# Performance work log

Measured on AMD Instinct MI355X. Metric: run time of the kernel, lower is better.

## Reference

```python
import jax, jax.numpy as jnp
import numpy as np

B, C, L, H = 2, 512, 4096, 8
D = C // H  # depth per head


def setup_inputs() -> dict:
    key = jax.random.key(0)
    k1, k2, k3 = jax.random.split(key, 3)
    queries = jax.random.normal(k1, (B, C, L), dtype=jnp.float32)
    mask = jnp.ones((B, L), dtype=jnp.int32)
    # xavier-ish scaling for stability
    Wm = jax.random.normal(k2, (2 * C, C), dtype=jnp.float32) * (1.0 / np.sqrt(C))
    Wq = jax.random.normal(k3, (C, C), dtype=jnp.float32) * (1.0 / np.sqrt(C))
    return {"queries": queries, "mask": mask, "Wm": Wm, "Wq": Wq}


def reference(queries, mask, Wm, Wq):
    # 1x1 conv projections == channel matmuls on [B, C, L]
    q = jnp.einsum('oc,bcl->bol', Wq, queries)   # [B, C, L]
    m = jnp.einsum('oc,bcl->bol', Wm, queries)   # [B, 2C, L]
    # to [B, L, *], split heads -> [B, H, L, D]
    qh = q.transpose(0, 2, 1).reshape(B, L, H, D).transpose(0, 2, 1, 3)
    mem = m.transpose(0, 2, 1)                   # [B, L, 2C]
    k, v = jnp.split(mem, 2, axis=2)             # each [B, L, C]
    kh = k.reshape(B, L, H, D).transpose(0, 2, 1, 3)
    vh = v.reshape(B, L, H, D).transpose(0, 2, 1, 3)
    qh = qh * (D ** -0.5)
    logits = jnp.einsum('bhqd,bhkd->bhqk', qh, kh)          # [B, H, L, L]
    mf = mask.astype(jnp.float32)[:, None, None, :]          # [B, 1, 1, L]
    logits = logits + (-1e30) * (1.0 - mf)
    weights = jax.nn.softmax(logits, axis=-1)                # dropout is identity in eval
    out = jnp.einsum('bhqk,bhkd->bhqd', weights, vh)         # [B, H, L, D]
    # combine heads -> [B, L, C] -> [B, C, L]
    return out.transpose(0, 2, 1, 3).reshape(B, L, C).transpose(0, 2, 1)
```

## Files before the change

### kernel.cpp

```cpp
#include <hip/hip_runtime.h>

#define Bn 2
#define Cn 512
#define Ln 4096
#define Hn 8
#define Dn 64

typedef _Float16 f16;
typedef _Float16 h8 __attribute__((ext_vector_type(8)));
typedef _Float16 h4 __attribute__((ext_vector_type(4)));
typedef float f32x4 __attribute__((ext_vector_type(4)));
typedef float f32x16 __attribute__((ext_vector_type(16)));

#define MFMA32(a, b, c) __builtin_amdgcn_mfma_f32_16x16x32_f16(a, b, c, 0, 0, 0)
#define MFMA3216(a, b, c) __builtin_amdgcn_mfma_f32_32x32x16_f16(a, b, c, 0, 0, 0)
#define AS1(p) ((const __attribute__((address_space(1))) void*)(p))
#define AS3(p) ((__attribute__((address_space(3))) void*)(p))

__global__ __launch_bounds__(256) void k_transpose(const float* __restrict__ X,
                                                   f16* __restrict__ Xt) {
  int bid = blockIdx.x;
  int b  = bid >> 9;
  int r  = bid & 511;
  int lt = r >> 3, ct = r & 7;
  int l0 = lt << 6, c0 = ct << 6;
  __shared__ f16 t[64][66];
  int tid = threadIdx.x;
  int lx = tid & 63, cg = tid >> 6;
  const float* xb = X + ((size_t)b * Cn) * Ln;
#pragma unroll
  for (int rr = 0; rr < 16; ++rr) {
    int cl = cg * 16 + rr;
    t[lx][cl] = (f16)xb[(size_t)(c0 + cl) * Ln + l0 + lx];
  }
  __syncthreads();
  f16* xo = Xt + ((size_t)b * Ln + l0) * Cn + c0;
  int cx = tid & 63, lg = tid >> 6;
#pragma unroll
  for (int rr = 0; rr < 16; ++rr) {
    int ll = lg * 16 + rr;
    xo[(size_t)ll * Cn + cx] = t[ll][cx];
  }
}

__global__ __launch_bounds__(256) void k_proj(const float* __restrict__ Wq,
                                              const float* __restrict__ Wm,
                                              const f16* __restrict__ Xt,
                                              f16* __restrict__ Qd,
                                              f16* __restrict__ Kd,
                                              f16* __restrict__ Vv) {
  int bid = blockIdx.x;
  int b = bid / 384;
  int r = bid % 384;
  int mt = r >> 5, nt = r & 31;
  int o0 = mt << 7, l0 = nt << 7;
  __shared__ f16 a_lds[128][40];
  __shared__ f16 b_lds[128][40];
  int tid = threadIdx.x;
  int lane = tid & 63, w = tid >> 6;
  int wr = w >> 1, wc = w & 1;
  f32x4 acc[4][4] = {};

  int sr = tid >> 1;
  int scg = (tid & 1) << 4;
  int o_s = o0 + sr;
  const float* wrow = (o_s < 512) ? (Wq + (size_t)o_s * Cn)
                                  : (Wm + (size_t)(o_s - 512) * Cn);
  const f16* xrow = Xt + ((size_t)b * Ln + l0 + sr) * Cn;

  for (int kt = 0; kt < 16; ++kt) {
    int c0 = kt << 5;
    __syncthreads();
#pragma unroll
    for (int i = 0; i < 4; ++i) {
      float4 w4 = *(const float4*)(wrow + c0 + scg + 4 * i);
      h4 hh = { (f16)w4.x, (f16)w4.y, (f16)w4.z, (f16)w4.w };
      *(h4*)&a_lds[sr][scg + 4 * i] = hh;
    }
#pragma unroll
    for (int i = 0; i < 2; ++i)
      *(h8*)&b_lds[sr][scg + 8 * i] = *(const h8*)(xrow + c0 + scg + 8 * i);
    __syncthreads();

    h8 af[4], bf[4];
#pragma unroll
    for (int mi = 0; mi < 4; ++mi)
      af[mi] = *(const h8*)&a_lds[wr * 64 + mi * 16 + (lane & 15)][(lane >> 4) * 8];
#pragma unroll
    for (int ni = 0; ni < 4; ++ni)
      bf[ni] = *(const h8*)&b_lds[wc * 64 + ni * 16 + (lane & 15)][(lane >> 4) * 8];
#pragma unroll
    for (int mi = 0; mi < 4; ++mi)
#pragma unroll
      for (int ni = 0; ni < 4; ++ni)
        acc[mi][ni] = MFMA32(af[mi], bf[ni], acc[mi][ni]);
  }

  const float QSCALE = 0.18033688011112042f;
  int lrow = (lane >> 4) << 2;
  int lcol = lane & 15;
#pragma unroll
  for (int mi = 0; mi < 4; ++mi) {
    int ob = o0 + wr * 64 + mi * 16 + lrow;
#pragma unroll
    for (int ni = 0; ni < 4; ++ni) {
      int lc = l0 + wc * 64 + ni * 16 + lcol;
      f32x4 a = acc[mi][ni];
      if (ob < 512) {
        int h = ob >> 6, d = ob & 63;
        h4 hh = { (f16)(a[0] * QSCALE), (f16)(a[1] * QSCALE),
                  (f16)(a[2] * QSCALE), (f16)(a[3] * QSCALE) };
        *(h4*)&Qd[(((size_t)b * Hn + h) * Ln + lc) * Dn + d] = hh;
      } else if (ob < 1024) {
        int oc = ob - 512;
        int h = oc >> 6, d = oc & 63;
        h4 hh = { (f16)a[0], (f16)a[1], (f16)a[2], (f16)a[3] };
        *(h4*)&Kd[(((size_t)b * Hn + h) * Ln + lc) * Dn + d] = hh;
      } else {
        int oc = ob - 1024;
#pragma unroll
        for (int rr = 0; rr < 4; ++rr)
          Vv[((size_t)b * Cn + oc + rr) * Ln + lc] = (f16)a[rr];
      }
    }
  }
}

__global__ __launch_bounds__(256, 2) void k_attn(const f16* __restrict__ Qd,
                                                 const f16* __restrict__ Kd,
                                                 const f16* __restrict__ Vv,
                                                 const int* __restrict__ mask,
                                                 float* __restrict__ out) {
  int bid0 = blockIdx.x;
  int bid = (bid0 & 7) * 64 + (bid0 >> 3);
  int bh = bid >> 5, ib = bid & 31;
  int b = bh >> 3, h = bh & 7;
  int tid = threadIdx.x;
  int lane = tid & 63, w = tid >> 6;
  int il = lane & 31, hi = lane >> 5;

  __shared__ __align__(16) f16 kbuf[4][64 * 64];
  __shared__ __align__(16) f16 vbuf[4][64 * 64];

  int qb = ib * 128 + w * 32;
  const f16* qp = Qd + ((size_t)bh * Ln + qb + il) * Dn;
  h8 qreg[4];
#pragma unroll
  for (int dt = 0; dt < 4; ++dt)
    qreg[dt] = *(const h8*)(qp + dt * 16 + hi * 8);

  const int* mbase = mask + (size_t)b * Ln;
  unsigned long long flags;
  {
    const int4* mp = (const int4*)mbase + lane * 16;
    int ac = 1;
#pragma unroll
    for (int q = 0; q < 16; ++q) { int4 v = mp[q]; ac &= v.x & v.y & v.z & v.w; }
    flags = __ballot(ac == 1);
  }

  const f16* kbase = Kd + (size_t)bh * Ln * Dn;
  const f16* vbase = Vv + ((size_t)b * Cn + h * 64) * Ln;
  int koff[2], voff[2];
#pragma unroll
  for (int q = 0; q < 2; ++q) {
    int rr = w * 16 + q * 8 + (lane >> 3);
    int swz = (lane & 7) ^ (rr & 7);
    koff[q] = rr * 64 + swz * 8;
    voff[q] = rr * Ln + swz * 8;
  }

#define STAGE(bi, t)                                                            \
  {                                                                             \
    _Pragma("unroll")                                                           \
    for (int q = 0; q < 2; ++q) {                                               \
      __builtin_amdgcn_global_load_lds(AS1(kbase + (size_t)(t) * 4096 + koff[q]),\
                                       AS3(&kbuf[bi][(w * 16 + q * 8) * 64]),   \
                                       16, 0, 0);                               \
      __builtin_amdgcn_global_load_lds(AS1(vbase + (size_t)(t) * 64 + voff[q]), \
                                       AS3(&vbuf[bi][(w * 16 + q * 8) * 64]),   \
                                       16, 0, 0);                               \
    }                                                                           \
  }

  f32x16 acc0 = {}, acc1 = {};
  float mrow = -1e38f;
  float lsum = 0.f;
  int swz7 = il & 7;

#define QK_TILE(KL, SN0, SN1)                                    \
  {                                                              \
    const f16* kl_ = (KL);                                       \
    f32x16 z0 = {}, z1 = {};                                     \
    _Pragma("unroll")                                            \
    for (int dt = 0; dt < 4; ++dt) {                             \
      int c = ((dt * 2 + hi) ^ swz7) << 3;                       \
      h8 ak0 = *(const h8*)&kl_[il * 64 + c];                    \
      h8 ak1 = *(const h8*)&kl_[(32 + il) * 64 + c];             \
      z0 = MFMA3216(ak0, qreg[dt], z0);                          \
      z1 = MFMA3216(ak1, qreg[dt], z1);                          \
    }                                                            \
    SN0 = z0; SN1 = z1;                                          \
  }

#define MASK_FIX(tt, S0, S1)                                     \
  if (!((flags >> (tt)) & 1)) {                                  \
    _Pragma("unroll")                                            \
    for (int r = 0; r < 16; ++r) {                               \
      int j = (tt) * 64 + (r & 3) + 8 * (r >> 2) + 4 * hi;       \
      if (!mbase[j])      S0[r] = -3.0e4f;                       \
      if (!mbase[j + 32]) S1[r] = -3.0e4f;                       \
    }                                                            \
  }

#define SOFTMAX_PV(tt, S0, S1)                                                  \
  {                                                                             \
    float m0 = fmaxf(fmaxf(S0[0], S0[1]), fmaxf(S0[2], S0[3]));                 \
    float m1 = fmaxf(fmaxf(S0[4], S0[5]), fmaxf(S0[6], S0[7]));                 \
    float m2 = fmaxf(fmaxf(S0[8], S0[9]), fmaxf(S0[10], S0[11]));               \
    float m3 = fmaxf(fmaxf(S0[12], S0[13]), fmaxf(S0[14], S0[15]));             \
    float m4 = fmaxf(fmaxf(S1[0], S1[1]), fmaxf(S1[2], S1[3]));                 \
    float m5 = fmaxf(fmaxf(S1[4], S1[5]), fmaxf(S1[6], S1[7]));                 \
    float m6 = fmaxf(fmaxf(S1[8], S1[9]), fmaxf(S1[10], S1[11]));               \
    float m7 = fmaxf(fmaxf(S1[12], S1[13]), fmaxf(S1[14], S1[15]));             \
    float mx = fmaxf(fmaxf(fmaxf(m0, m1), fmaxf(m2, m3)),                       \
                     fmaxf(fmaxf(m4, m5), fmaxf(m6, m7)));                      \
    mx = fmaxf(mx, __shfl_xor(mx, 32));                                         \
    if (__any(mx > mrow + 8.f)) {                     \
      float mn = fmaxf(mrow, mx);                                               \
      float al = __builtin_amdgcn_exp2f(mrow - mn);                             \
      lsum *= al;                                                               \
      _Pragma("unroll")                                                         \
      for (int r = 0; r < 16; ++r) { acc0[r] *= al; acc1[r] *= al; }            \
      mrow = mn;                                                                \
    }                                                                           \
    _Pragma("unroll")                                                           \
    for (int r = 0; r < 16; ++r) {                                              \
      S0[r] = __builtin_amdgcn_exp2f(S0[r] - mrow);                             \
      S1[r] = __builtin_amdgcn_exp2f(S1[r] - mrow);                             \
    }                                                                           \
    {                                           \
      float a0 = (S0[0] + S0[1]) + (S0[2] + S0[3]);                             \
      float a1 = (S0[4] + S0[5]) + (S0[6] + S0[7]);                             \
      float a2 = (S0[8] + S0[9]) + (S0[10] + S0[11]);                           \
      float a3 = (S0[12] + S0[13]) + (S0[14] + S0[15]);                         \
      float a4 = (S1[0] + S1[1]) + (S1[2] + S1[3]);                             \
      float a5 = (S1[4] + S1[5]) + (S1[6] + S1[7]);                             \
      float a6 = (S1[8] + S1[9]) + (S1[10] + S1[11]);                           \
      float a7 = (S1[12] + S1[13]) + (S1[14] + S1[15]);                         \
      float rs = ((a0 + a1) + (a2 + a3)) + ((a4 + a5) + (a6 + a7));             \
      rs += __shfl_xor(rs, 32);                                                 \
      lsum += rs;                                                               \
    }                                                                           \
    float dw0[8], dw1[8];                                                       \
    _Pragma("unroll")                                                           \
    for (int r = 0; r < 16; r += 2) {                                           \
      dw0[r >> 1] = __builtin_bit_cast(float,                                   \
          __builtin_amdgcn_cvt_pkrtz(S0[r], S0[r + 1]));                        \
      dw1[r >> 1] = __builtin_bit_cast(float,                                   \
          __builtin_amdgcn_cvt_pkrtz(S1[r], S1[r + 1]));                        \
    }                                                                           \
    h8 pb[4];                                                                   \
    _Pragma("unroll")                                                           \
    for (int jt = 0; jt < 4; ++jt) {                                            \
      const float* dd = (jt < 2) ? dw0 : dw1;                                   \
      int base = (jt & 1) * 4;                                                  \
      float x0 = dd[base + 0], x1 = dd[base + 1];                               \
      float y0 = dd[base + 2], y1 = dd[base + 3];                               \
      float v0 = hi ? x0 : y0, v1 = hi ? x1 : y1;                               \
      float p0 = __shfl_xor(v0, 32), p1 = __shfl_xor(v1, 32);                   \
      union { h8 v; float f[4]; } u;                                            \
      u.f[0] = hi ? p0 : x0;                                                    \
      u.f[1] = hi ? p1 : x1;                                                    \
      u.f[2] = hi ? y0 : p0;                                                    \
      u.f[3] = hi ? y1 : p1;                                                    \
      pb[jt] = u.v;                                                             \
    }                                                                           \
    const f16* vl_ = &vbuf[(tt) & 3][0];                                        \
    __builtin_amdgcn_s_setprio(1);                                              \
    _Pragma("unroll")                                                           \
    for (int dt = 0; dt < 2; ++dt) {                                            \
      int rv = dt * 32 + il;                                                    \
      _Pragma("unroll")                                                         \
      for (int jt = 0; jt < 4; ++jt) {                                          \
        h8 av = *(const h8*)&vl_[rv * 64 + (((jt * 2 + hi) ^ swz7) << 3)];      \
        if (dt == 0) acc0 = MFMA3216(av, pb[jt], acc0);                         \
        else         acc1 = MFMA3216(av, pb[jt], acc1);                         \
      }                                                                         \
    }                                                                           \
    __builtin_amdgcn_s_setprio(0);                                              \
  }

#define BODY(tt, SC0, SC1, SN0, SN1)                                            \
  {                                                                             \
    asm volatile("s_waitcnt vmcnt(4)" ::: "memory");                            \
    __builtin_amdgcn_s_barrier();                                               \
    if ((tt) + 3 < 64) STAGE(((tt) + 3) & 3, (tt) + 3);                         \
    QK_TILE(&kbuf[((tt) + 1) & 3][0], SN0, SN1);                                \
    MASK_FIX((tt) + 1, SN0, SN1);                                               \
    SOFTMAX_PV(tt, SC0, SC1);                                                   \
  }

  STAGE(0, 0);
  STAGE(1, 1);
  STAGE(2, 2);
  asm volatile("s_waitcnt vmcnt(8)" ::: "memory");
  __builtin_amdgcn_s_barrier();
  f32x16 sE0, sE1, sO0, sO1;
  QK_TILE(&kbuf[0][0], sE0, sE1);
  MASK_FIX(0, sE0, sE1);

  for (int t = 0; t < 62; t += 2) {
    BODY(t, sE0, sE1, sO0, sO1);
    BODY(t + 1, sO0, sO1, sE0, sE1);
  }
  {
    asm volatile("s_waitcnt vmcnt(0)" ::: "memory");
    __builtin_amdgcn_s_barrier();
    QK_TILE(&kbuf[3][0], sO0, sO1);
    MASK_FIX(63, sO0, sO1);
    SOFTMAX_PV(62, sE0, sE1);
  }
  SOFTMAX_PV(63, sO0, sO1);

  float inv = 1.f / lsum;
  size_t obase = ((size_t)b * Cn + h * 64) * Ln + qb + il;
#pragma unroll
  for (int r = 0; r < 16; ++r) {
    int d0 = (r & 3) + 8 * (r >> 2) + 4 * hi;
    out[obase + (size_t)d0 * Ln] = acc0[r] * inv;
    out[obase + (size_t)(d0 + 32) * Ln] = acc1[r] * inv;
  }
}

extern "C" void kernel_launch(void* const* d_in, const int* in_sizes, int n_in,
                              void* d_out, int out_size, void* d_ws, size_t ws_size,
                              hipStream_t stream) {
  const float* queries = (const float*)d_in[0];
  const int*   mask    = (const int*)d_in[1];
  const float* Wm      = (const float*)d_in[2];
  const float* Wq      = (const float*)d_in[3];
  float* out = (float*)d_out;
  char* ws = (char*)d_ws;
  f16* Xt = (f16*)(ws);
  f16* Qd = (f16*)(ws + 8388608);
  f16* Kd = (f16*)(ws + 16777216);
  f16* Vv = (f16*)(ws + 25165824);

  k_transpose<<<1024, 256, 0, stream>>>(queries, Xt);
  k_proj<<<768, 256, 0, stream>>>(Wq, Wm, Xt, Qd, Kd, Vv);
  k_attn<<<512, 256, 0, stream>>>(Qd, Kd, Vv, mask, out);
}
```

Baseline: 145.6 us.

## Split KV range across two wave groups per block and merge softmax partials

```diff
diff --git a/kernel.cpp b/kernel.cpp
--- a/kernel.cpp
+++ b/kernel.cpp
@@ -126,7 +126,7 @@
   }
 }
 
-__global__ __launch_bounds__(256, 2) void k_attn(const f16* __restrict__ Qd,
+__global__ __launch_bounds__(512, 4) void k_attn(const f16* __restrict__ Qd,
                                                  const f16* __restrict__ Kd,
                                                  const f16* __restrict__ Vv,
                                                  const int* __restrict__ mask,
@@ -137,12 +137,14 @@
   int b = bh >> 3, h = bh & 7;
   int tid = threadIdx.x;
   int lane = tid & 63, w = tid >> 6;
+  int grp = w >> 2, wq = w & 3;
   int il = lane & 31, hi = lane >> 5;
 
-  __shared__ __align__(16) f16 kbuf[4][64 * 64];
-  __shared__ __align__(16) f16 vbuf[4][64 * 64];
-
-  int qb = ib * 128 + w * 32;
+  __shared__ __align__(16) f16 smem[8 * 4096];
+#define KBUF(g, bi) (&smem[(((g) * 2 + (bi))) * 4096])
+#define VBUF(g, bi) (&smem[((4 + (g) * 2 + (bi))) * 4096])
+
+  int qb = ib * 128 + wq * 32;
   const f16* qp = Qd + ((size_t)bh * Ln + qb + il) * Dn;
   h8 qreg[4];
 #pragma unroll
@@ -159,12 +161,12 @@
     flags = __ballot(ac == 1);
   }
 
-  const f16* kbase = Kd + (size_t)bh * Ln * Dn;
-  const f16* vbase = Vv + ((size_t)b * Cn + h * 64) * Ln;
+  const f16* kbase = Kd + (size_t)bh * Ln * Dn + (size_t)grp * 32 * 4096;
+  const f16* vbase = Vv + ((size_t)b * Cn + h * 64) * Ln + grp * 32 * 64;
   int koff[2], voff[2];
 #pragma unroll
   for (int q = 0; q < 2; ++q) {
-    int rr = w * 16 + q * 8 + (lane >> 3);
+    int rr = wq * 16 + q * 8 + (lane >> 3);
     int swz = (lane & 7) ^ (rr & 7);
     koff[q] = rr * 64 + swz * 8;
     voff[q] = rr * Ln + swz * 8;
@@ -175,10 +177,10 @@
     _Pragma("unroll")                                                           \
     for (int q = 0; q < 2; ++q) {                                               \
       __builtin_amdgcn_global_load_lds(AS1(kbase + (size_t)(t) * 4096 + koff[q]),\
-                                       AS3(&kbuf[bi][(w * 16 + q * 8) * 64]),   \
+                                       AS3(KBUF(grp, bi) + (wq * 16 + q * 8) * 64),\
                                        16, 0, 0);                               \
       __builtin_amdgcn_global_load_lds(AS1(vbase + (size_t)(t) * 64 + voff[q]), \
-                                       AS3(&vbuf[bi][(w * 16 + q * 8) * 64]),   \
+                                       AS3(VBUF(grp, bi) + (wq * 16 + q * 8) * 64),\
                                        16, 0, 0);                               \
     }                                                                           \
   }
@@ -188,41 +190,42 @@
   float lsum = 0.f;
   int swz7 = il & 7;
 
-#define QK_TILE(KL, SN0, SN1)                                    \
-  {                                                              \
-    const f16* kl_ = (KL);                                       \
-    f32x16 z0 = {}, z1 = {};                                     \
-    _Pragma("unroll")                                            \
-    for (int dt = 0; dt < 4; ++dt) {                             \
-      int c = ((dt * 2 + hi) ^ swz7) << 3;                       \
-      h8 ak0 = *(const h8*)&kl_[il * 64 + c];                    \
-      h8 ak1 = *(const h8*)&kl_[(32 + il) * 64 + c];             \
-      z0 = MFMA3216(ak0, qreg[dt], z0);                          \
-      z1 = MFMA3216(ak1, qreg[dt], z1);                          \
-    }                                                            \
-    SN0 = z0; SN1 = z1;                                          \
-  }
-
-#define MASK_FIX(tt, S0, S1)                                     \
-  if (!((flags >> (tt)) & 1)) {                                  \
-    _Pragma("unroll")                                            \
-    for (int r = 0; r < 16; ++r) {                               \
-      int j = (tt) * 64 + (r & 3) + 8 * (r >> 2) + 4 * hi;       \
-      if (!mbase[j])      S0[r] = -3.0e4f;                       \
-      if (!mbase[j + 32]) S1[r] = -3.0e4f;                       \
-    }                                                            \
-  }
-
-#define SOFTMAX_PV(tt, S0, S1)                                                  \
+  STAGE(0, 0);
+  STAGE(1, 1);
+
+#define BODY(t_, waitn_)                                                        \
   {                                                                             \
-    float m0 = fmaxf(fmaxf(S0[0], S0[1]), fmaxf(S0[2], S0[3]));                 \
-    float m1 = fmaxf(fmaxf(S0[4], S0[5]), fmaxf(S0[6], S0[7]));                 \
-    float m2 = fmaxf(fmaxf(S0[8], S0[9]), fmaxf(S0[10], S0[11]));               \
-    float m3 = fmaxf(fmaxf(S0[12], S0[13]), fmaxf(S0[14], S0[15]));             \
-    float m4 = fmaxf(fmaxf(S1[0], S1[1]), fmaxf(S1[2], S1[3]));                 \
-    float m5 = fmaxf(fmaxf(S1[4], S1[5]), fmaxf(S1[6], S1[7]));                 \
-    float m6 = fmaxf(fmaxf(S1[8], S1[9]), fmaxf(S1[10], S1[11]));               \
-    float m7 = fmaxf(fmaxf(S1[12], S1[13]), fmaxf(S1[14], S1[15]));             \
+    asm volatile("s_waitcnt vmcnt(" waitn_ ")" ::: "memory");                   \
+    __builtin_amdgcn_s_barrier();                                               \
+    const f16* kl_ = KBUF(grp, (t_) & 1);                                       \
+    f32x16 s0 = {}, s1 = {};                                                    \
+    __builtin_amdgcn_s_setprio(1);                                              \
+    _Pragma("unroll")                                                           \
+    for (int dt = 0; dt < 4; ++dt) {                                            \
+      int c = ((dt * 2 + hi) ^ swz7) << 3;                                      \
+      h8 ak0 = *(const h8*)&kl_[il * 64 + c];                                   \
+      h8 ak1 = *(const h8*)&kl_[(32 + il) * 64 + c];                            \
+      s0 = MFMA3216(ak0, qreg[dt], s0);                                         \
+      s1 = MFMA3216(ak1, qreg[dt], s1);                                         \
+    }                                                                           \
+    __builtin_amdgcn_s_setprio(0);                                              \
+    int T_ = grp * 32 + (t_);                                                   \
+    if (!((flags >> T_) & 1)) {                                                 \
+      _Pragma("unroll")                                                         \
+      for (int r = 0; r < 16; ++r) {                                            \
+        int j = T_ * 64 + (r & 3) + 8 * (r >> 2) + 4 * hi;                      \
+        if (!mbase[j])      s0[r] = -3.0e4f;                                    \
+        if (!mbase[j + 32]) s1[r] = -3.0e4f;                                    \
+      }                                                                         \
+    }                                                                           \
+    float m0 = fmaxf(fmaxf(s0[0], s0[1]), fmaxf(s0[2], s0[3]));                 \
+    float m1 = fmaxf(fmaxf(s0[4], s0[5]), fmaxf(s0[6], s0[7]));                 \
+    float m2 = fmaxf(fmaxf(s0[8], s0[9]), fmaxf(s0[10], s0[11]));               \
+    float m3 = fmaxf(fmaxf(s0[12], s0[13]), fmaxf(s0[14], s0[15]));             \
+    float m4 = fmaxf(fmaxf(s1[0], s1[1]), fmaxf(s1[2], s1[3]));                 \
+    float m5 = fmaxf(fmaxf(s1[4], s1[5]), fmaxf(s1[6], s1[7]));                 \
+    float m6 = fmaxf(fmaxf(s1[8], s1[9]), fmaxf(s1[10], s1[11]));               \
+    float m7 = fmaxf(fmaxf(s1[12], s1[13]), fmaxf(s1[14], s1[15]));             \
     float mx = fmaxf(fmaxf(fmaxf(m0, m1), fmaxf(m2, m3)),                       \
                      fmaxf(fmaxf(m4, m5), fmaxf(m6, m7)));                      \
     mx = fmaxf(mx, __shfl_xor(mx, 32));                                         \
@@ -236,18 +239,18 @@
     }                                                                           \
     _Pragma("unroll")                                                           \
     for (int r = 0; r < 16; ++r) {                                              \
-      S0[r] = __builtin_amdgcn_exp2f(S0[r] - mrow);                             \
-      S1[r] = __builtin_amdgcn_exp2f(S1[r] - mrow);                             \
-    }                                                                           \
-    {                                           \
-      float a0 = (S0[0] + S0[1]) + (S0[2] + S0[3]);                             \
-      float a1 = (S0[4] + S0[5]) + (S0[6] + S0[7]);                             \
-      float a2 = (S0[8] + S0[9]) + (S0[10] + S0[11]);                           \
-      float a3 = (S0[12] + S0[13]) + (S0[14] + S0[15]);                         \
-      float a4 = (S1[0] + S1[1]) + (S1[2] + S1[3]);                             \
-      float a5 = (S1[4] + S1[5]) + (S1[6] + S1[7]);                             \
-      float a6 = (S1[8] + S1[9]) + (S1[10] + S1[11]);                           \
-      float a7 = (S1[12] + S1[13]) + (S1[14] + S1[15]);                         \
+      s0[r] = __builtin_amdgcn_exp2f(s0[r] - mrow);                             \
+      s1[r] = __builtin_amdgcn_exp2f(s1[r] - mrow);                             \
+    }                                                                           \
+    {                                                    \
+      float a0 = (s0[0] + s0[1]) + (s0[2] + s0[3]);                             \
+      float a1 = (s0[4] + s0[5]) + (s0[6] + s0[7]);                             \
+      float a2 = (s0[8] + s0[9]) + (s0[10] + s0[11]);                           \
+      float a3 = (s0[12] + s0[13]) + (s0[14] + s0[15]);                         \
+      float a4 = (s1[0] + s1[1]) + (s1[2] + s1[3]);                             \
+      float a5 = (s1[4] + s1[5]) + (s1[6] + s1[7]);                             \
+      float a6 = (s1[8] + s1[9]) + (s1[10] + s1[11]);                           \
+      float a7 = (s1[12] + s1[13]) + (s1[14] + s1[15]);                         \
       float rs = ((a0 + a1) + (a2 + a3)) + ((a4 + a5) + (a6 + a7));             \
       rs += __shfl_xor(rs, 32);                                                 \
       lsum += rs;                                                               \
@@ -256,9 +259,9 @@
     _Pragma("unroll")                                                           \
     for (int r = 0; r < 16; r += 2) {                                           \
       dw0[r >> 1] = __builtin_bit_cast(float,                                   \
-          __builtin_amdgcn_cvt_pkrtz(S0[r], S0[r + 1]));                        \
+          __builtin_amdgcn_cvt_pkrtz(s0[r], s0[r + 1]));                        \
       dw1[r >> 1] = __builtin_bit_cast(float,                                   \
-          __builtin_amdgcn_cvt_pkrtz(S1[r], S1[r + 1]));                        \
+          __builtin_amdgcn_cvt_pkrtz(s1[r], s1[r + 1]));                        \
     }                                                                           \
     h8 pb[4];                                                                   \
     _Pragma("unroll")                                                           \
@@ -276,7 +279,7 @@
       u.f[3] = hi ? y1 : p1;                                                    \
       pb[jt] = u.v;                                                             \
     }                                                                           \
-    const f16* vl_ = &vbuf[(tt) & 3][0];                                        \
+    const f16* vl_ = VBUF(grp, (t_) & 1);                                       \
     __builtin_amdgcn_s_setprio(1);                                              \
     _Pragma("unroll")                                                           \
     for (int dt = 0; dt < 2; ++dt) {                                            \
@@ -289,47 +292,41 @@
       }                                                                         \
     }                                                                           \
     __builtin_amdgcn_s_setprio(0);                                              \
-  }
-
-#define BODY(tt, SC0, SC1, SN0, SN1)                                            \
-  {                                                                             \
-    asm volatile("s_waitcnt vmcnt(4)" ::: "memory");                            \
     __builtin_amdgcn_s_barrier();                                               \
-    if ((tt) + 3 < 64) STAGE(((tt) + 3) & 3, (tt) + 3);                         \
-    QK_TILE(&kbuf[((tt) + 1) & 3][0], SN0, SN1);                                \
-    MASK_FIX((tt) + 1, SN0, SN1);                                               \
-    SOFTMAX_PV(tt, SC0, SC1);                                                   \
-  }
-
-  STAGE(0, 0);
-  STAGE(1, 1);
-  STAGE(2, 2);
-  asm volatile("s_waitcnt vmcnt(8)" ::: "memory");
-  __builtin_amdgcn_s_barrier();
-  f32x16 sE0, sE1, sO0, sO1;
-  QK_TILE(&kbuf[0][0], sE0, sE1);
-  MASK_FIX(0, sE0, sE1);
-
-  for (int t = 0; t < 62; t += 2) {
-    BODY(t, sE0, sE1, sO0, sO1);
-    BODY(t + 1, sO0, sO1, sE0, sE1);
-  }
-  {
-    asm volatile("s_waitcnt vmcnt(0)" ::: "memory");
-    __builtin_amdgcn_s_barrier();
-    QK_TILE(&kbuf[3][0], sO0, sO1);
-    MASK_FIX(63, sO0, sO1);
-    SOFTMAX_PV(62, sE0, sE1);
-  }
-  SOFTMAX_PV(63, sO0, sO1);
-
-  float inv = 1.f / lsum;
-  size_t obase = ((size_t)b * Cn + h * 64) * Ln + qb + il;
-#pragma unroll
-  for (int r = 0; r < 16; ++r) {
-    int d0 = (r & 3) + 8 * (r >> 2) + 4 * hi;
-    out[obase + (size_t)d0 * Ln] = acc0[r] * inv;
-    out[obase + (size_t)(d0 + 32) * Ln] = acc1[r] * inv;
+    if ((t_) < 30) STAGE((t_) & 1, (t_) + 2);                                   \
+  }
+
+  for (int t = 0; t < 31; ++t) {
+    BODY(t, "4");
+  }
+  BODY(31, "0");
+
+  __syncthreads();
+  float* shf = (float*)smem;
+  if (grp == 1) {
+    float* basep = shf + wq * (64 * 33) + lane * 33;
+#pragma unroll
+    for (int r = 0; r < 16; ++r) { basep[r] = acc0[r]; basep[16 + r] = acc1[r]; }
+    float* ml = shf + 4 * 64 * 33 + (wq * 64 + lane) * 2;
+    ml[0] = mrow; ml[1] = lsum;
+  }
+  __syncthreads();
+  if (grp == 0) {
+    float* basep = shf + wq * (64 * 33) + lane * 33;
+    float* ml = shf + 4 * 64 * 33 + (wq * 64 + lane) * 2;
+    float mB = ml[0], lB = ml[1];
+    float M = fmaxf(mrow, mB);
+    float wA = __builtin_amdgcn_exp2f(mrow - M);
+    float wB = __builtin_amdgcn_exp2f(mB - M);
+    float linv = 1.f / (lsum * wA + lB * wB);
+    float fA = wA * linv, fB = wB * linv;
+    size_t obase = ((size_t)b * Cn + h * 64) * Ln + qb + il;
+#pragma unroll
+    for (int r = 0; r < 16; ++r) {
+      int d0 = (r & 3) + 8 * (r >> 2) + 4 * hi;
+      out[obase + (size_t)d0 * Ln] = acc0[r] * fA + basep[r] * fB;
+      out[obase + (size_t)(d0 + 32) * Ln] = acc1[r] * fA + basep[16 + r] * fB;
+    }
   }
 }
 
@@ -349,5 +346,5 @@
 
   k_transpose<<<1024, 256, 0, stream>>>(queries, Xt);
   k_proj<<<768, 256, 0, stream>>>(Wq, Wm, Xt, Qd, Kd, Vv);
-  k_attn<<<512, 256, 0, stream>>>(Qd, Kd, Vv, mask, out);
+  k_attn<<<512, 512, 0, stream>>>(Qd, Kd, Vv, mask, out);
 }
```

After: 140.6 us. 3.5% less time.
